# Optimization experiments

Measured on AMD Instinct MI355X. Metric: run time of the kernel, lower is better.

The kernel has to match this reference:

```python
import jax, jax.numpy as jnp
import numpy as np


def setup_inputs() -> dict:
    key = jax.random.key(0)
    kq, kk, kv = jax.random.split(key, 3)
    B, H, N, D = 2, 16, 2048, 128
    q = jax.random.normal(kq, (B, H, N, D), dtype=jnp.float32)
    k = jax.random.normal(kk, (B, H, N, D), dtype=jnp.float32)
    v = jax.random.normal(kv, (B, H, N, D), dtype=jnp.float32)
    return {"q": q, "k": k, "v": v, "num_sink": 4, "window_size": 1024}


def reference(q, k, v, num_sink, window_size):
    # Sink + sliding-window causal attention (single-device path of the SP wrapper).
    # Query i attends to key j iff j <= i AND (j < num_sink OR i - j < window_size).
    B, H, N, D = q.shape
    scale = 1.0 / np.sqrt(D).astype(np.float32)
    i = jnp.arange(N)[:, None]   # query positions
    j = jnp.arange(N)[None, :]   # key positions
    mask = (j <= i) & ((j < num_sink) | ((i - j) < window_size))  # [N, N]
    scores = jnp.einsum('bhid,bhjd->bhij', q, k) * scale          # [B,H,N,N]
    scores = jnp.where(mask, scores, jnp.finfo(scores.dtype).min)
    attn = jax.nn.softmax(scores, axis=-1)
    return jnp.einsum('bhij,bhjd->bhid', attn, v)
```

## Files before the change

### kernel.cpp

```cpp
#include <hip/hip_runtime.h>
#include <stdint.h>

#define NN 2048
#define DD 128
#define BHH 32
#define QT 64
#define KT 64

typedef short v8s __attribute__((ext_vector_type(8)));
typedef short v4s __attribute__((ext_vector_type(4)));
typedef float v4f __attribute__((ext_vector_type(4)));
typedef float v16f __attribute__((ext_vector_type(16)));
typedef unsigned int u32;
typedef u32 u32x2 __attribute__((ext_vector_type(2)));
typedef u32 u32x4 __attribute__((ext_vector_type(4)));

__device__ __forceinline__ unsigned short f2bf(float x) {
  unsigned u = __builtin_bit_cast(unsigned, x);
  u += 0x7fffu + ((u >> 16) & 1u);
  return (unsigned short)(u >> 16);
}

__device__ __forceinline__ v8s cvt8(const float* __restrict__ p) {
  v8s r;
#pragma unroll
  for (int j = 0; j < 8; j++) r[j] = (short)f2bf(p[j]);
  return r;
}

__device__ __forceinline__ u32 pk2(float a, float b) {
  u32 r;
  asm("v_cvt_pk_bf16_f32 %0, %1, %2" : "=v"(r) : "v"(a), "v"(b));
  return r;
}

__device__ __forceinline__ void gl_lds16(const unsigned short* g, unsigned short* l) {
  __builtin_amdgcn_global_load_lds((const unsigned int*)g, (unsigned int*)l, 16, 0, 0);
}

__global__ __launch_bounds__(256) void prep(const float* __restrict__ K, const float* __restrict__ V,
                     unsigned short* __restrict__ Kb, unsigned short* __restrict__ Vt) {
  const int z = blockIdx.z;
  const int tid = threadIdx.x;
  if (z >= BHH) {
    const int bh = z - BHH;
    const int kb32 = blockIdx.y * 32 + blockIdx.x;
    const int m = tid & 31, kc = tid >> 5;
    const float* src = K + ((size_t)bh * NN + kb32 * 32 + m) * DD + kc * 16;
    v4f a0 = *(const v4f*)(src);
    v4f a1 = *(const v4f*)(src + 4);
    v4f a2 = *(const v4f*)(src + 8);
    v4f a3 = *(const v4f*)(src + 12);
    u32x4 w0 = { pk2(a0[0], a0[1]), pk2(a0[2], a0[3]), pk2(a1[0], a1[1]), pk2(a1[2], a1[3]) };
    u32x4 w1 = { pk2(a2[0], a2[1]), pk2(a2[2], a2[3]), pk2(a3[0], a3[1]), pk2(a3[2], a3[3]) };
    unsigned short* base = Kb + (((size_t)bh * 64 + kb32) * 8 + kc) * 512;
    *(u32x4*)(base + (size_t)m * 8) = w0;
    *(u32x4*)(base + (size_t)(32 + m) * 8) = w1;
    return;
  }
  __shared__ __align__(16) unsigned short t[64 * 68];
  const int bh = z;
  const int n0b = blockIdx.x, d0b = blockIdx.y;
  const int c16 = tid & 15, r4 = tid >> 4;
  const float* src = V + ((size_t)bh * NN + n0b * 64 + r4 * 4) * DD + d0b * 64 + c16 * 4;
  v4f f0 = *(const v4f*)(src);
  v4f f1 = *(const v4f*)(src + DD);
  v4f f2 = *(const v4f*)(src + 2 * DD);
  v4f f3 = *(const v4f*)(src + 3 * DD);
#pragma unroll
  for (int j = 0; j < 4; j++) {
    u32x2 w = { pk2(f0[j], f1[j]), pk2(f2[j], f3[j]) };
    *(u32x2*)(t + (c16 * 4 + j) * 68 + r4 * 4) = w;
  }
  __syncthreads();
  unsigned short* Vfb = Vt + (size_t)bh * (512u * 512);
#pragma unroll
  for (int p = 0; p < 2; p++) {
    const int fid = p * 4 + (tid >> 6);
    const int ktl = fid >> 1, ncl = fid & 1;
    const int lane = tid & 63;
    const int dloc = ncl * 32 + (lane & 31);
    const int nloc = ktl * 16 + (lane >> 5) * 8;
    v4s x0 = *(const v4s*)(t + dloc * 68 + nloc);
    v4s x1 = *(const v4s*)(t + dloc * 68 + nloc + 4);
    v8s o = { x0[0], x0[1], x0[2], x0[3], x1[0], x1[1], x1[2], x1[3] };
    const size_t fi = (size_t)(n0b * 4 + ktl) * 4 + (d0b * 2 + ncl);
    *(v8s*)(Vfb + fi * 512 + (size_t)lane * 8) = o;
  }
}

template <bool PREPPED>
__global__ __launch_bounds__(128) __attribute__((amdgpu_waves_per_eu(1, 2)))
void attn(
    const float* __restrict__ Q,
    const float* __restrict__ Kf, const unsigned short* __restrict__ Kb,
    const unsigned short* __restrict__ Vfr, const float* __restrict__ Vf,
    const int* __restrict__ nsp, const int* __restrict__ wsp,
    float* __restrict__ O) {
  const int ns = nsp[0], win = wsp[0];
  const int x = blockIdx.x;
  const int xcd = x & 7, slot = x >> 3;
  const int bh = xcd + 8 * (slot / 24);
  const int jobid = slot % 24;
  int qis[2], njobs;
  if (jobid < 16) { njobs = 1; qis[0] = 31 - jobid; qis[1] = 0; }
  else { int p = jobid - 16; njobs = 2; qis[0] = 15 - p; qis[1] = p; }

  const int tid = threadIdx.x;
  const int w = tid >> 6;
  const int l = tid & 63;
  const int m = l & 31;
  const int hi = l >> 5;
  const int rbase = 4 * hi;

  __shared__ __align__(16) unsigned short Kl[2][16 * 512];

  const float csc = 0.088388347648318447f * 1.4426950408889634f;

  const unsigned short* Vfb = Vfr + (size_t)bh * (512u * 512);

  auto mkpa = [&](float a0, float a1, float a2, float a3,
                  float b0, float b1, float b2, float b3) -> v8s {
    u32x2 r02 = __builtin_amdgcn_permlane32_swap(pk2(a0, a1), pk2(b0, b1), false, false);
    u32x2 r13 = __builtin_amdgcn_permlane32_swap(pk2(a2, a3), pk2(b2, b3), false, false);
    u32x4 pw = { r02[0], r13[0], r02[1], r13[1] };
    return __builtin_bit_cast(v8s, pw);
  };

  for (int ji = 0; ji < njobs; ji++) {
    const int q0 = qis[ji] * QT;
    const int qrow0w = q0 + w * 32;
    const int qi = qrow0w + m;

    v8s qf[8];
    {
      const float* qb = Q + ((size_t)bh * NN + qi) * DD + hi * 8;
#pragma unroll
      for (int kc = 0; kc < 8; kc++) {
        v4f a = *(const v4f*)(qb + kc * 16);
        v4f b = *(const v4f*)(qb + kc * 16 + 4);
        u32x4 pw = { pk2(a[0] * csc, a[1] * csc), pk2(a[2] * csc, a[3] * csc),
                     pk2(b[0] * csc, b[1] * csc), pk2(b[2] * csc, b[3] * csc) };
        qf[kc] = __builtin_bit_cast(v8s, pw);
      }
    }

    float lsum = 0.f;
    v16f oa[4];
#pragma unroll
    for (int nc = 0; nc < 4; nc++) oa[nc] = (v16f)(0.f);

    const int wstart = q0 - win + 1;
    const bool sink16 = (wstart > KT - 1) && (ns <= 16);
    const int kb_lo = sink16 ? ((wstart >> 6) << 6) : 0;
    const int kb_hi = q0 + QT;

    if constexpr (PREPPED) {
      auto issueK = [&](int kb, int buf) {
        const unsigned short* src =
            Kb + (((size_t)bh * 64 + (kb >> 5) + w) * 8) * 512 + (size_t)l * 8;
        unsigned short* dst = &Kl[buf][(w * 8) * 512];
#pragma unroll
        for (int i = 0; i < 8; i++)
          gl_lds16(src + (size_t)i * 512, dst + i * 512);
      };

      int cur = 0;
      issueK(kb_lo, 0);

      if (sink16) {
        v8s kf0[8];
#pragma unroll
        for (int kc = 0; kc < 8; kc++)
          kf0[kc] = *(const v8s*)(Kb + ((size_t)bh * 64 * 8 + kc) * 512 + (size_t)l * 8);
        v16f s = (v16f)(0.f);
#pragma unroll
        for (int kc = 0; kc < 8; kc++)
          s = __builtin_amdgcn_mfma_f32_32x32x16_bf16(kf0[kc], qf[kc], s, 0, 0, 0);
#pragma unroll
        for (int reg = 0; reg < 16; reg++) {
          const int kj = (reg & 3) + 8 * (reg >> 2) + rbase;
          const bool valid = (kj < ns) && (kj <= qi);
          s[reg] = valid ? __builtin_amdgcn_exp2f(s[reg]) : 0.f;
        }
        lsum += (((s[0] + s[1]) + (s[2] + s[3])) + ((s[4] + s[5]) + (s[6] + s[7])))
              + (((s[8] + s[9]) + (s[10] + s[11])) + ((s[12] + s[13]) + (s[14] + s[15])));
        v8s pa = mkpa(s[0], s[1], s[2], s[3], s[4], s[5], s[6], s[7]);
#pragma unroll
        for (int nc = 0; nc < 4; nc++) {
          v8s vf = *(const v8s*)(Vfb + (size_t)nc * 512 + (size_t)l * 8);
          oa[nc] = __builtin_amdgcn_mfma_f32_32x32x16_bf16(pa, vf, oa[nc], 0, 0, 0);
        }
      }

      asm volatile("s_waitcnt vmcnt(0)" ::: "memory");
      __syncthreads();

      for (int kb = kb_lo; kb < kb_hi; kb += KT) {
        if (kb + KT < kb_hi) issueK(kb + KT, cur ^ 1);
        v8s vf[16];
#pragma unroll
        for (int i = 0; i < 16; i++) {
          const int kt = i >> 2, nc = i & 3;
          vf[i] = *(const v8s*)(Vfb + ((size_t)((kb >> 4) + kt) * 4 + nc) * 512 + (size_t)l * 8);
        }

#pragma unroll
        for (int ct = 0; ct < 2; ct++) {
          v16f s = (v16f)(0.f);
          __builtin_amdgcn_s_setprio(1);
#pragma unroll
          for (int kc = 0; kc < 8; kc++) {
            v8s kfr = *(const v8s*)(&Kl[cur][(ct * 8 + kc) * 512 + l * 8]);
            s = __builtin_amdgcn_mfma_f32_32x32x16_bf16(kfr, qf[kc], s, 0, 0, 0);
          }
          __builtin_amdgcn_s_setprio(0);

          const int kbct = kb + ct * 32;
          const bool full = (kbct + 31 <= qrow0w) && (kbct >= qrow0w + 32 - win);
          if (full) {
#pragma unroll
            for (int reg = 0; reg < 16; reg++) s[reg] = __builtin_amdgcn_exp2f(s[reg]);
          } else {
#pragma unroll
            for (int reg = 0; reg < 16; reg++) {
              const int kj = kbct + (reg & 3) + 8 * (reg >> 2) + rbase;
              const bool valid = (kj <= qi) && ((kj < ns) || (qi - kj < win));
              s[reg] = valid ? __builtin_amdgcn_exp2f(s[reg]) : 0.f;
            }
          }
          lsum += (((s[0] + s[1]) + (s[2] + s[3])) + ((s[4] + s[5]) + (s[6] + s[7])))
                + (((s[8] + s[9]) + (s[10] + s[11])) + ((s[12] + s[13]) + (s[14] + s[15])));

          v8s pa0 = mkpa(s[0], s[1], s[2], s[3], s[4], s[5], s[6], s[7]);
          v8s pa1 = mkpa(s[8], s[9], s[10], s[11], s[12], s[13], s[14], s[15]);

          __builtin_amdgcn_s_setprio(1);
#pragma unroll
          for (int ktl = 0; ktl < 2; ktl++) {
            const v8s pf = ktl ? pa1 : pa0;
#pragma unroll
            for (int nc = 0; nc < 4; nc++)
              oa[nc] = __builtin_amdgcn_mfma_f32_32x32x16_bf16(pf, vf[(ct * 2 + ktl) * 4 + nc],
                                                               oa[nc], 0, 0, 0);
          }
          __builtin_amdgcn_s_setprio(0);
        }

        asm volatile("s_waitcnt vmcnt(0)" ::: "memory");
        __syncthreads();
        cur ^= 1;
      }
    } else {
      for (int kb = 0; kb < kb_hi; kb += KT) {
        if ((kb >= ns) && (kb + KT - 1 < wstart)) continue;
#pragma unroll
        for (int ct = 0; ct < 2; ct++) {
          v16f s = (v16f)(0.f);
#pragma unroll
          for (int kc = 0; kc < 8; kc++) {
            v8s kfr = cvt8(Kf + ((size_t)bh * NN + kb + ct * 32 + m) * DD + kc * 16 + hi * 8);
            s = __builtin_amdgcn_mfma_f32_32x32x16_bf16(kfr, qf[kc], s, 0, 0, 0);
          }
#pragma unroll
          for (int reg = 0; reg < 16; reg++) {
            const int kj = kb + ct * 32 + (reg & 3) + 8 * (reg >> 2) + rbase;
            const bool valid = (kj <= qi) && ((kj < ns) || (qi - kj < win));
            s[reg] = valid ? __builtin_amdgcn_exp2f(s[reg]) : 0.f;
            lsum += s[reg];
          }
          v8s pa0 = mkpa(s[0], s[1], s[2], s[3], s[4], s[5], s[6], s[7]);
          v8s pa1 = mkpa(s[8], s[9], s[10], s[11], s[12], s[13], s[14], s[15]);
#pragma unroll
          for (int ktl = 0; ktl < 2; ktl++) {
            const v8s pf = ktl ? pa1 : pa0;
#pragma unroll
            for (int nc = 0; nc < 4; nc++) {
              v8s vfe;
#pragma unroll
              for (int e = 0; e < 8; e++)
                vfe[e] = (short)f2bf(Vf[((size_t)bh * NN + kb + (ct * 2 + ktl) * 16 + hi * 8 + e) * DD + nc * 32 + m]);
              oa[nc] = __builtin_amdgcn_mfma_f32_32x32x16_bf16(pf, vfe, oa[nc], 0, 0, 0);
            }
          }
        }
      }
    }

    float lt = lsum + __shfl_xor(lsum, 32, 64);
    const float inv = 1.f / lt;
    float* ob = O + ((size_t)bh * NN + qrow0w) * DD;
#pragma unroll
    for (int reg = 0; reg < 16; reg++) {
      const int row = (reg & 3) + 8 * (reg >> 2) + rbase;
      const float iv = __shfl(inv, row, 64);
#pragma unroll
      for (int nc = 0; nc < 4; nc++)
        ob[(size_t)row * DD + nc * 32 + m] = oa[nc][reg] * iv;
    }
  }
}

extern "C" void kernel_launch(void* const* d_in, const int* in_sizes, int n_in,
                              void* d_out, int out_size, void* d_ws, size_t ws_size,
                              hipStream_t stream) {
  const float* q = (const float*)d_in[0];
  const float* k = (const float*)d_in[1];
  const float* v = (const float*)d_in[2];
  const int* nsp = (const int*)d_in[3];
  const int* wsp = (const int*)d_in[4];
  float* out = (float*)d_out;

  const size_t half = (size_t)BHH * NN * DD * sizeof(unsigned short);
  const int nblocks = BHH * 24;

  if (ws_size >= 2 * half) {
    unsigned short* kfrag = (unsigned short*)d_ws;
    unsigned short* vfrag = (unsigned short*)((char*)d_ws + half);
    prep<<<dim3(32, 2, 2 * BHH), 256, 0, stream>>>(k, v, kfrag, vfrag);
    attn<true><<<nblocks, 128, 0, stream>>>(q, k, kfrag, vfrag, v, nsp, wsp, out);
  } else {
    attn<false><<<nblocks, 128, 0, stream>>>(q, k, nullptr, nullptr, v, nsp, wsp, out);
  }
}
```

Measured before the change: 191.0 us.

## Split each query tile's key range across two blocks and merge partials

Each 64-row query tile's key range is divided into two halves handled by separate blocks (a split-K style flash-decoding scheme). One half writes unnormalized fp32 output, the other writes bf16 partials, and both write row sums. A merge kernel then combines them and normalizes. This replaces the old paired-job load balancing with uniform split work and more blocks (2048), at the cost of extra global traffic, a third kernel launch and bf16 rounding of half the partial output. Launch bounds also change from a waves-per-EU hint to a minimum of 2 blocks.

```diff
diff --git a/kernel.cpp b/kernel.cpp
--- a/kernel.cpp
+++ b/kernel.cpp
@@ -19,13 +19,6 @@
   unsigned u = __builtin_bit_cast(unsigned, x);
   u += 0x7fffu + ((u >> 16) & 1u);
   return (unsigned short)(u >> 16);
-}
-
-__device__ __forceinline__ v8s cvt8(const float* __restrict__ p) {
-  v8s r;
-#pragma unroll
-  for (int j = 0; j < 8; j++) r[j] = (short)f2bf(p[j]);
-  return r;
 }
 
 __device__ __forceinline__ u32 pk2(float a, float b) {
@@ -89,22 +82,28 @@
   }
 }
 
-template <bool PREPPED>
-__global__ __launch_bounds__(128) __attribute__((amdgpu_waves_per_eu(1, 2)))
-void attn(
-    const float* __restrict__ Q,
-    const float* __restrict__ Kf, const unsigned short* __restrict__ Kb,
-    const unsigned short* __restrict__ Vfr, const float* __restrict__ Vf,
+template <bool SPLIT>
+__global__ __launch_bounds__(128, 2) void attn(
+    const float* __restrict__ Q, const unsigned short* __restrict__ Kb,
+    const unsigned short* __restrict__ Vfr,
     const int* __restrict__ nsp, const int* __restrict__ wsp,
-    float* __restrict__ O) {
+    float* __restrict__ O, unsigned short* __restrict__ pB,
+    float* __restrict__ lsA, float* __restrict__ lsB) {
   const int ns = nsp[0], win = wsp[0];
   const int x = blockIdx.x;
-  const int xcd = x & 7, slot = x >> 3;
-  const int bh = xcd + 8 * (slot / 24);
-  const int jobid = slot % 24;
-  int qis[2], njobs;
-  if (jobid < 16) { njobs = 1; qis[0] = 31 - jobid; qis[1] = 0; }
-  else { int p = jobid - 16; njobs = 2; qis[0] = 15 - p; qis[1] = p; }
+  int bh, hf = 0, qis[2], njobs;
+  if constexpr (SPLIT) {
+    const int xcd = x & 7, r = x >> 3;
+    bh = xcd + 8 * (r >> 6);
+    const int inner = r & 63;
+    qis[0] = inner >> 1; qis[1] = 0; hf = inner & 1; njobs = 1;
+  } else {
+    const int xcd = x & 7, slot = x >> 3;
+    bh = xcd + 8 * (slot / 24);
+    const int jobid = slot % 24;
+    if (jobid < 16) { njobs = 1; qis[0] = 31 - jobid; qis[1] = 0; }
+    else { int p = jobid - 16; njobs = 2; qis[0] = 15 - p; qis[1] = p; }
+  }
 
   const int tid = threadIdx.x;
   const int w = tid >> 6;
@@ -151,53 +150,61 @@
     for (int nc = 0; nc < 4; nc++) oa[nc] = (v16f)(0.f);
 
     const int wstart = q0 - win + 1;
-    const bool sink16 = (wstart > KT - 1) && (ns <= 16);
-    const int kb_lo = sink16 ? ((wstart >> 6) << 6) : 0;
+    const bool sink16_all = (wstart > KT - 1) && (ns <= 16);
+    const int kb_lo = sink16_all ? ((wstart >> 6) << 6) : 0;
     const int kb_hi = q0 + QT;
-
-    if constexpr (PREPPED) {
-      auto issueK = [&](int kb, int buf) {
-        const unsigned short* src =
-            Kb + (((size_t)bh * 64 + (kb >> 5) + w) * 8) * 512 + (size_t)l * 8;
-        unsigned short* dst = &Kl[buf][(w * 8) * 512];
-#pragma unroll
-        for (int i = 0; i < 8; i++)
-          gl_lds16(src + (size_t)i * 512, dst + i * 512);
-      };
-
-      int cur = 0;
-      issueK(kb_lo, 0);
-
-      if (sink16) {
-        v8s kf0[8];
-#pragma unroll
-        for (int kc = 0; kc < 8; kc++)
-          kf0[kc] = *(const v8s*)(Kb + ((size_t)bh * 64 * 8 + kc) * 512 + (size_t)l * 8);
-        v16f s = (v16f)(0.f);
-#pragma unroll
-        for (int kc = 0; kc < 8; kc++)
-          s = __builtin_amdgcn_mfma_f32_32x32x16_bf16(kf0[kc], qf[kc], s, 0, 0, 0);
-#pragma unroll
-        for (int reg = 0; reg < 16; reg++) {
-          const int kj = (reg & 3) + 8 * (reg >> 2) + rbase;
-          const bool valid = (kj < ns) && (kj <= qi);
-          s[reg] = valid ? __builtin_amdgcn_exp2f(s[reg]) : 0.f;
-        }
-        lsum += (((s[0] + s[1]) + (s[2] + s[3])) + ((s[4] + s[5]) + (s[6] + s[7])))
-              + (((s[8] + s[9]) + (s[10] + s[11])) + ((s[12] + s[13]) + (s[14] + s[15])));
-        v8s pa = mkpa(s[0], s[1], s[2], s[3], s[4], s[5], s[6], s[7]);
-#pragma unroll
-        for (int nc = 0; nc < 4; nc++) {
-          v8s vf = *(const v8s*)(Vfb + (size_t)nc * 512 + (size_t)l * 8);
-          oa[nc] = __builtin_amdgcn_mfma_f32_32x32x16_bf16(pa, vf, oa[nc], 0, 0, 0);
-        }
-      }
-
+    int kb_begin = kb_lo, kb_end = kb_hi;
+    bool do_sink = sink16_all;
+    if constexpr (SPLIT) {
+      const int T = (kb_hi - kb_lo) >> 6;
+      const int TA = (T + 1) >> 1;
+      if (hf == 0) { kb_end = kb_lo + TA * KT; do_sink = false; }
+      else         { kb_begin = kb_lo + TA * KT; }
+    }
+
+    auto issueK = [&](int kb, int buf) {
+      const unsigned short* src =
+          Kb + (((size_t)bh * 64 + (kb >> 5) + w) * 8) * 512 + (size_t)l * 8;
+      unsigned short* dst = &Kl[buf][(w * 8) * 512];
+#pragma unroll
+      for (int i = 0; i < 8; i++)
+        gl_lds16(src + (size_t)i * 512, dst + i * 512);
+    };
+
+    const bool haveloop = kb_begin < kb_end;
+    if (haveloop) issueK(kb_begin, 0);
+
+    if (do_sink) {
+      v8s kf0[8];
+#pragma unroll
+      for (int kc = 0; kc < 8; kc++)
+        kf0[kc] = *(const v8s*)(Kb + ((size_t)bh * 64 * 8 + kc) * 512 + (size_t)l * 8);
+      v16f s = (v16f)(0.f);
+#pragma unroll
+      for (int kc = 0; kc < 8; kc++)
+        s = __builtin_amdgcn_mfma_f32_32x32x16_bf16(kf0[kc], qf[kc], s, 0, 0, 0);
+#pragma unroll
+      for (int reg = 0; reg < 16; reg++) {
+        const int kj = (reg & 3) + 8 * (reg >> 2) + rbase;
+        const bool valid = (kj < ns) && (kj <= qi);
+        s[reg] = valid ? __builtin_amdgcn_exp2f(s[reg]) : 0.f;
+      }
+      lsum += (((s[0] + s[1]) + (s[2] + s[3])) + ((s[4] + s[5]) + (s[6] + s[7])))
+            + (((s[8] + s[9]) + (s[10] + s[11])) + ((s[12] + s[13]) + (s[14] + s[15])));
+      v8s pa = mkpa(s[0], s[1], s[2], s[3], s[4], s[5], s[6], s[7]);
+#pragma unroll
+      for (int nc = 0; nc < 4; nc++) {
+        v8s vf = *(const v8s*)(Vfb + (size_t)nc * 512 + (size_t)l * 8);
+        oa[nc] = __builtin_amdgcn_mfma_f32_32x32x16_bf16(pa, vf, oa[nc], 0, 0, 0);
+      }
+    }
+
+    if (haveloop) {
       asm volatile("s_waitcnt vmcnt(0)" ::: "memory");
       __syncthreads();
-
-      for (int kb = kb_lo; kb < kb_hi; kb += KT) {
-        if (kb + KT < kb_hi) issueK(kb + KT, cur ^ 1);
+      int cur = 0;
+      for (int kb = kb_begin; kb < kb_end; kb += KT) {
+        if (kb + KT < kb_end) issueK(kb + KT, cur ^ 1);
         v8s vf[16];
 #pragma unroll
         for (int i = 0; i < 16; i++) {
@@ -251,53 +258,62 @@
         __syncthreads();
         cur ^= 1;
       }
+    }
+
+    float lt = lsum + __shfl_xor(lsum, 32, 64);
+    if constexpr (SPLIT) {
+      if (hf == 0) {
+        float* ob = O + ((size_t)bh * NN + qrow0w) * DD;
+#pragma unroll
+        for (int reg = 0; reg < 16; reg++) {
+          const int row = (reg & 3) + 8 * (reg >> 2) + rbase;
+#pragma unroll
+          for (int nc = 0; nc < 4; nc++)
+            ob[(size_t)row * DD + nc * 32 + m] = oa[nc][reg];
+        }
+        if (hi == 0) lsA[((size_t)bh << 11) + qrow0w + m] = lt;
+      } else {
+        unsigned short* pb = pB + ((size_t)bh * NN + qrow0w) * DD;
+#pragma unroll
+        for (int reg = 0; reg < 16; reg++) {
+          const int row = (reg & 3) + 8 * (reg >> 2) + rbase;
+#pragma unroll
+          for (int nc = 0; nc < 4; nc++)
+            pb[(size_t)row * DD + nc * 32 + m] = f2bf(oa[nc][reg]);
+        }
+        if (hi == 0) lsB[((size_t)bh << 11) + qrow0w + m] = lt;
+      }
     } else {
-      for (int kb = 0; kb < kb_hi; kb += KT) {
-        if ((kb >= ns) && (kb + KT - 1 < wstart)) continue;
-#pragma unroll
-        for (int ct = 0; ct < 2; ct++) {
-          v16f s = (v16f)(0.f);
-#pragma unroll
-          for (int kc = 0; kc < 8; kc++) {
-            v8s kfr = cvt8(Kf + ((size_t)bh * NN + kb + ct * 32 + m) * DD + kc * 16 + hi * 8);
-            s = __builtin_amdgcn_mfma_f32_32x32x16_bf16(kfr, qf[kc], s, 0, 0, 0);
-          }
-#pragma unroll
-          for (int reg = 0; reg < 16; reg++) {
-            const int kj = kb + ct * 32 + (reg & 3) + 8 * (reg >> 2) + rbase;
-            const bool valid = (kj <= qi) && ((kj < ns) || (qi - kj < win));
-            s[reg] = valid ? __builtin_amdgcn_exp2f(s[reg]) : 0.f;
-            lsum += s[reg];
-          }
-          v8s pa0 = mkpa(s[0], s[1], s[2], s[3], s[4], s[5], s[6], s[7]);
-          v8s pa1 = mkpa(s[8], s[9], s[10], s[11], s[12], s[13], s[14], s[15]);
-#pragma unroll
-          for (int ktl = 0; ktl < 2; ktl++) {
-            const v8s pf = ktl ? pa1 : pa0;
-#pragma unroll
-            for (int nc = 0; nc < 4; nc++) {
-              v8s vfe;
-#pragma unroll
-              for (int e = 0; e < 8; e++)
-                vfe[e] = (short)f2bf(Vf[((size_t)bh * NN + kb + (ct * 2 + ktl) * 16 + hi * 8 + e) * DD + nc * 32 + m]);
-              oa[nc] = __builtin_amdgcn_mfma_f32_32x32x16_bf16(pf, vfe, oa[nc], 0, 0, 0);
-            }
-          }
-        }
-      }
-    }
-
-    float lt = lsum + __shfl_xor(lsum, 32, 64);
-    const float inv = 1.f / lt;
-    float* ob = O + ((size_t)bh * NN + qrow0w) * DD;
-#pragma unroll
-    for (int reg = 0; reg < 16; reg++) {
-      const int row = (reg & 3) + 8 * (reg >> 2) + rbase;
-      const float iv = __shfl(inv, row, 64);
-#pragma unroll
-      for (int nc = 0; nc < 4; nc++)
-        ob[(size_t)row * DD + nc * 32 + m] = oa[nc][reg] * iv;
-    }
+      const float inv = 1.f / lt;
+      float* ob = O + ((size_t)bh * NN + qrow0w) * DD;
+#pragma unroll
+      for (int reg = 0; reg < 16; reg++) {
+        const int row = (reg & 3) + 8 * (reg >> 2) + rbase;
+        const float iv = __shfl(inv, row, 64);
+#pragma unroll
+        for (int nc = 0; nc < 4; nc++)
+          ob[(size_t)row * DD + nc * 32 + m] = oa[nc][reg] * iv;
+      }
+    }
+  }
+}
+
+__global__ __launch_bounds__(256) void merge(float* __restrict__ O,
+    const unsigned short* __restrict__ pB, const float* __restrict__ lsA,
+    const float* __restrict__ lsB) {
+  const int total4 = BHH * NN * DD / 4;
+  for (int i = blockIdx.x * 256 + threadIdx.x; i < total4; i += gridDim.x * 256) {
+    v4f o = ((const v4f*)O)[i];
+    v4s b = ((const v4s*)pB)[i];
+    const int row = i >> 5;
+    const float inv = 1.f / (lsA[row] + lsB[row]);
+    v4f r;
+#pragma unroll
+    for (int j = 0; j < 4; j++) {
+      const float bf = __builtin_bit_cast(float, (u32)((unsigned short)b[j]) << 16);
+      r[j] = (o[j] + bf) * inv;
+    }
+    ((v4f*)O)[i] = r;
   }
 }
 
@@ -311,15 +327,22 @@
   const int* wsp = (const int*)d_in[4];
   float* out = (float*)d_out;
 
-  const size_t half = (size_t)BHH * NN * DD * sizeof(unsigned short);
-  const int nblocks = BHH * 24;
-
-  if (ws_size >= 2 * half) {
-    unsigned short* kfrag = (unsigned short*)d_ws;
-    unsigned short* vfrag = (unsigned short*)((char*)d_ws + half);
+  const size_t MB16 = 16777216;
+  const size_t LS = (size_t)BHH * NN * 4;
+  char* ws = (char*)d_ws;
+  unsigned short* kfrag = (unsigned short*)ws;
+  unsigned short* vfrag = (unsigned short*)(ws + MB16);
+
+  if (ws_size >= 3 * MB16 + 2 * LS) {
+    unsigned short* pB = (unsigned short*)(ws + 2 * MB16);
+    float* lsA = (float*)(ws + 3 * MB16);
+    float* lsB = (float*)(ws + 3 * MB16 + LS);
     prep<<<dim3(32, 2, 2 * BHH), 256, 0, stream>>>(k, v, kfrag, vfrag);
-    attn<true><<<nblocks, 128, 0, stream>>>(q, k, kfrag, vfrag, v, nsp, wsp, out);
+    attn<true><<<2048, 128, 0, stream>>>(q, kfrag, vfrag, nsp, wsp, out, pB, lsA, lsB);
+    merge<<<2048, 256, 0, stream>>>(out, pB, lsA, lsB);
   } else {
-    attn<false><<<nblocks, 128, 0, stream>>>(q, k, nullptr, nullptr, v, nsp, wsp, out);
-  }
-}
+    prep<<<dim3(32, 2, 2 * BHH), 256, 0, stream>>>(k, v, kfrag, vfrag);
+    attn<false><<<BHH * 24, 128, 0, stream>>>(q, kfrag, vfrag, nsp, wsp, out,
+                                              nullptr, nullptr, nullptr);
+  }
+}
```

Measured after the change: 194.2 us. No clear change (+1.7%).
